# Kernel tuning notes

Hardware: AMD Instinct MI355X
Metric: run time of the kernel (lower is better)

The kernel has to match this reference:

```python
import jax, jax.numpy as jnp
import numpy as np

TINY = 1e-15
EPS = 1e-6
B, T, D, H, N = 1, 512, 512, 8, 64
A = N + 1  # ambient dim
TAU = 1.0


def mink(x, y):
    # Minkowski inner product over the last dim
    return -x[..., 0] * y[..., 0] + jnp.sum(x[..., 1:] * y[..., 1:], axis=-1)


def project(x):
    xx = mink(x, x)
    scale = jnp.sqrt(jnp.maximum(jnp.abs(xx), TINY))[..., None]
    x = x / scale
    return jnp.concatenate([jnp.abs(x[..., :1]), x[..., 1:]], axis=-1)


def exp_map(p, v):
    vn = jnp.sqrt(jnp.maximum(mink(v, v), TINY))[..., None]
    y = jnp.cosh(vn) * p + (jnp.sinh(vn) / jnp.maximum(vn, TINY)) * v
    return project(y)


def log_map(p, y):
    alpha = -mink(p, y)
    dist = jnp.arccosh(jnp.maximum(alpha, 1.0 + EPS))[..., None]
    u = y + alpha[..., None] * p
    un = jnp.sqrt(jnp.maximum(mink(u, u), TINY))[..., None]
    return dist / jnp.maximum(un, TINY) * u


def rope(u):
    # u: [B,H,T,N]; standard half-rotation RoPE, base 10000
    inv_freq = 1.0 / (10000.0 ** (jnp.arange(0, N, 2, dtype=jnp.float32) / N))
    ang = jnp.arange(T, dtype=jnp.float32)[:, None] * inv_freq[None, :]  # [T, N/2]
    cos = jnp.concatenate([jnp.cos(ang), jnp.cos(ang)], axis=-1)  # [T, N]
    sin = jnp.concatenate([jnp.sin(ang), jnp.sin(ang)], axis=-1)
    u1, u2 = u[..., : N // 2], u[..., N // 2:]
    rot = jnp.concatenate([-u2, u1], axis=-1)
    return u * cos + rot * sin


def lift(u):
    # append time-like 0, expmap at origin -> points on hyperboloid [B,H,T,A]
    v = jnp.concatenate([jnp.zeros(u.shape[:-1] + (1,), u.dtype), u], axis=-1)
    o = jnp.zeros((A,), u.dtype).at[0].set(1.0)
    return exp_map(o, v)


def setup_inputs() -> dict:
    key = jax.random.key(0)
    ks = jax.random.split(key, 10)
    s = 0.02
    x = jax.random.normal(ks[0], (B, T, D), jnp.float32)
    Wq = jax.random.normal(ks[1], (D, H * N), jnp.float32) * s
    bq = jax.random.normal(ks[2], (H * N,), jnp.float32) * s
    Wk = jax.random.normal(ks[3], (D, H * N), jnp.float32) * s
    bk = jax.random.normal(ks[4], (H * N,), jnp.float32) * s
    Wv = jax.random.normal(ks[5], (D, H * N), jnp.float32) * s
    bv = jax.random.normal(ks[6], (H * N,), jnp.float32) * s
    Wo = jax.random.normal(ks[7], (H * A, D), jnp.float32) * s
    bo = jax.random.normal(ks[8], (D,), jnp.float32) * s
    sp = jax.random.normal(ks[9], (N,), jnp.float32) * 0.1
    anchor_p = jnp.concatenate([jnp.sqrt(1.0 + jnp.sum(sp * sp))[None], sp])  # valid hyperboloid point
    return dict(x=x, Wq=Wq, bq=bq, Wk=Wk, bk=bk, Wv=Wv, bv=bv, Wo=Wo, bo=bo, anchor_p=anchor_p)


def reference(x, Wq, bq, Wk, bk, Wv, bv, Wo, bo, anchor_p):
    def pack(u):  # [B,T,H*N] -> [B,H,T,N]
        return u.reshape(B, T, H, N).transpose(0, 2, 1, 3)

    uq = rope(pack(x @ Wq + bq))
    uk = rope(pack(x @ Wk + bk))
    uv = pack(x @ Wv + bv)
    Q = lift(uq)  # [B,H,T,A]
    K = lift(uk)
    V = lift(uv)

    # pairwise Lorentz distance scores, softmax in fp32
    alpha_qk = -mink(Q[:, :, :, None, :].astype(jnp.float32), K[:, :, None, :, :].astype(jnp.float32))
    d = jnp.arccosh(jnp.maximum(alpha_qk, 1.0 + EPS))  # [B,H,T,T]
    attn = jax.nn.softmax(-TAU * d * d, axis=-1).astype(V.dtype)

    # one Karcher-mean step around the query point (karcher_steps=1)
    Y = Q
    logv = log_map(Y[:, :, :, None, :], V[:, :, None, :, :])  # [B,H,T,T,A]
    u = jnp.sum(attn[..., None] * logv, axis=3)  # [B,H,T,A]
    Y = exp_map(Y, u)

    Yc = Y.transpose(0, 2, 1, 3)  # [B,T,H,A]
    Z_tan = log_map(anchor_p[None, None, None, :], Yc).reshape(B, T, H * A)
    return Z_tan @ Wo + bo
```

## Files before the change

### kernel.cpp

```cpp
#include <hip/hip_runtime.h>
#include <math.h>

#define T_ 512
#define D_ 512
#define H_ 8
#define N_ 64
#define A_ 65
#define HN_ 512
#define HA_ 520
#define QS_ 66
#define VS_ 66
#define KTS_ 512
#define SYS_ 68
#define EPS_ 1e-6
#define EPSF_ 1e-6f
#define TINY_ 1e-15
#define IT 8
#define PTT 4
#define CTT 2

__device__ __forceinline__ double wsumd(double v){
#pragma unroll
  for (int o=32;o;o>>=1) v += __shfl_xor(v,o);
  return v;
}
__device__ __forceinline__ float wsumf(float v){
#pragma unroll
  for (int o=32;o;o>>=1) v += __shfl_xor(v,o);
  return v;
}
__device__ __forceinline__ float wmaxf(float v){
#pragma unroll
  for (int o=32;o;o>>=1) v = fmaxf(v,__shfl_xor(v,o));
  return v;
}
__device__ __forceinline__ float facoshf(float x){
  return __logf(x + sqrtf(fmaf(x,x,-1.f)));
}

__global__ void k_fill(float* __restrict__ out, float val){
  int i = blockIdx.x*256 + threadIdx.x;
  if (i < T_*D_) out[i] = val;
}

__global__ __launch_bounds__(256) void k_projlift(
    const float* __restrict__ x,
    const float* __restrict__ Wq, const float* __restrict__ bq,
    const float* __restrict__ Wk, const float* __restrict__ bk,
    const float* __restrict__ Wv, const float* __restrict__ bv,
    double* __restrict__ Qd, float* __restrict__ KTf,
    float* __restrict__ Vf, float* __restrict__ VTf){
  int mode = blockIdx.y;
  const float* W  = (mode==0)?Wq:((mode==1)?Wk:Wv);
  const float* bb = (mode==0)?bq:((mode==1)?bk:bv);
  int tid = threadIdx.x;
  int c = blockIdx.x*256 + tid;
  int n = c & 63, h = c >> 6;
  int t0 = blockIdx.z*PTT;
  float acc[PTT];
#pragma unroll
  for (int i=0;i<PTT;i++) acc[i]=0.f;

  float w0[8], w1[8];
#pragma unroll
  for (int k=0;k<8;k++) w0[k] = W[(size_t)(k)*HN_ + c];
#pragma unroll
  for (int k=0;k<8;k++) w1[k] = W[(size_t)(8+k)*HN_ + c];

#pragma unroll 2
  for (int d=0; d<D_-16; d+=8){
    float wp[8];
#pragma unroll
    for (int k=0;k<8;k++) wp[k] = W[(size_t)(d+16+k)*HN_ + c];
#pragma unroll
    for (int i=0;i<PTT;i++){
      const float* xr = x + (size_t)(t0+i)*D_ + d;
#pragma unroll
      for (int k=0;k<8;k++) acc[i] = fmaf(xr[k], w0[k], acc[i]);
    }
#pragma unroll
    for (int k=0;k<8;k++){ w0[k]=w1[k]; w1[k]=wp[k]; }
  }
#pragma unroll
  for (int i=0;i<PTT;i++){
    const float* xr = x + (size_t)(t0+i)*D_ + (D_-16);
#pragma unroll
    for (int k=0;k<8;k++) acc[i] = fmaf(xr[k],   w0[k], acc[i]);
#pragma unroll
    for (int k=0;k<8;k++) acc[i] = fmaf(xr[8+k], w1[k], acc[i]);
  }

  float bias = bb[c];
  double inv_f = 0.0;
  if (mode < 2) inv_f = 1.0 / pow(10000.0, (double)(2*(n&31))*(1.0/64.0));
#pragma unroll 1
  for (int i=0;i<PTT;i++){
    int t = t0 + i;
    double v = (double)(acc[i] + bias);
    if (mode < 2){
      double ang = (double)t * inv_f;
      double vp = __shfl_xor(v, 32);
      double rot = (n<32) ? -vp : vp;
      v = v*cos(ang) + rot*sin(ang);
    }
    double ss = wsumd(v*v);
    double vn = sqrt(fmax(ss, TINY_));
    double ch = cosh(vn);
    double s  = sinh(vn)/fmax(vn, TINY_);
    double y  = s*v;
    double xx = wsumd(y*y) - ch*ch;
    double scale = sqrt(fmax(fabs(xx), TINY_));
    double y0 = fabs(ch/scale), ya = y/scale;
    if (mode==0){
      double* o = Qd + (size_t)h*T_*QS_ + (size_t)t*QS_;
      if (n==0) o[0] = y0;
      o[n+1] = ya;
    } else if (mode==1){
      float* o = KTf + (size_t)h*66*KTS_ + t;
      if (n==0) o[0] = (float)y0;
      o[(size_t)(n+1)*KTS_] = (float)ya;
    } else {
      float y0f = (float)y0, yaf = (float)ya;
      float* o = Vf + (size_t)h*T_*VS_ + (size_t)t*VS_;
      if (n==0) o[0] = y0f;
      o[n+1] = yaf;
      float* ot = VTf + (size_t)h*66*KTS_ + t;
      if (n==0) ot[0] = y0f;
      ot[(size_t)(n+1)*KTS_] = yaf;
    }
  }
}

__global__ __launch_bounds__(256) void k_attnF(
    const double* __restrict__ Qd, const float* __restrict__ KTf,
    const float* __restrict__ VTf, const float* __restrict__ Vf,
    const float* __restrict__ anchor, float* __restrict__ Z){
  __shared__ double sYd[IT][QS_];
  __shared__ float  sYm[IT][SYS_];
  __shared__ float  s_w[IT][T_];
  __shared__ double sA[A_];
  __shared__ float  s_red[4][IT];
  __shared__ float  s_part[4][IT][64];
  __shared__ float  s_p64[4][IT];

  int h = blockIdx.x, i0 = blockIdx.y*IT, tid = threadIdx.x;
  int wv = tid>>6, lane = tid&63;
  const double* Qp = Qd  + (size_t)h*T_*QS_;
  const float*  KT = KTf + (size_t)h*66*KTS_;
  const float*  VT = VTf + (size_t)h*66*KTS_;
  const float*  Vp = Vf  + (size_t)h*T_*VS_;

  for (int f=tid; f<IT*QS_; f+=256){
    int i=f/QS_, a=f-i*QS_;
    sYd[i][a] = (a<A_) ? Qp[(size_t)(i0+i)*QS_ + a] : 0.0;
  }
  for (int f=tid; f<IT*SYS_; f+=256){
    int i=f/SYS_, a=f-i*SYS_;
    float v = (a<A_) ? (float)Qp[(size_t)(i0+i)*QS_ + a] : 0.f;
    sYm[i][a] = (a==0) ? v : -v;
  }
  if (tid < A_) sA[tid] = (double)anchor[tid];
  __syncthreads();

  int j0 = tid, j1 = tid + 256;
  {
    float aq0[IT], aq1[IT];
#pragma unroll
    for (int i=0;i<IT;i++){ aq0[i]=0.f; aq1[i]=0.f; }
    for (int a4=0; a4<16; a4++){
      int a = a4*4;
      float k00=KT[(size_t)(a+0)*KTS_+j0], k01=KT[(size_t)(a+1)*KTS_+j0];
      float k02=KT[(size_t)(a+2)*KTS_+j0], k03=KT[(size_t)(a+3)*KTS_+j0];
      float k10=KT[(size_t)(a+0)*KTS_+j1], k11=KT[(size_t)(a+1)*KTS_+j1];
      float k12=KT[(size_t)(a+2)*KTS_+j1], k13=KT[(size_t)(a+3)*KTS_+j1];
#pragma unroll
      for (int i=0;i<IT;i++){
        float4 ym = *reinterpret_cast<const float4*>(&sYm[i][a]);
        aq0[i] = fmaf(ym.w,k03,fmaf(ym.z,k02,fmaf(ym.y,k01,fmaf(ym.x,k00,aq0[i]))));
        aq1[i] = fmaf(ym.w,k13,fmaf(ym.z,k12,fmaf(ym.y,k11,fmaf(ym.x,k10,aq1[i]))));
      }
    }
    float kt0 = KT[(size_t)64*KTS_+j0], kt1 = KT[(size_t)64*KTS_+j1];
#pragma unroll
    for (int i=0;i<IT;i++){
      float a0 = fmaf(sYm[i][64], kt0, aq0[i]);
      float a1 = fmaf(sYm[i][64], kt1, aq1[i]);
      float d0 = facoshf(fmaxf(a0, 1.f+EPSF_));
      float d1 = facoshf(fmaxf(a1, 1.f+EPSF_));
      s_w[i][j0] = -d0*d0;
      s_w[i][j1] = -d1*d1;
    }
  }
  __syncthreads();

  for (int ii=0; ii<2; ii++){
    int i = wv*2 + ii;
    float m = -INFINITY;
#pragma unroll
    for (int kk=0;kk<8;kk++) m = fmaxf(m, s_w[i][lane+64*kk]);
    m = wmaxf(m);
    float e[8], sum=0.f;
#pragma unroll
    for (int kk=0;kk<8;kk++){ e[kk]=__expf(s_w[i][lane+64*kk]-m); sum+=e[kk]; }
    sum = wsumf(sum);
    float inv = 1.f/sum;
#pragma unroll
    for (int kk=0;kk<8;kk++) s_w[i][lane+64*kk] = e[kk]*inv;
  }
  __syncthreads();

  {
    float av0[IT], av1[IT];
#pragma unroll
    for (int i=0;i<IT;i++){ av0[i]=0.f; av1[i]=0.f; }
    for (int a4=0; a4<16; a4++){
      int a = a4*4;
      float v00=VT[(size_t)(a+0)*KTS_+j0], v01=VT[(size_t)(a+1)*KTS_+j0];
      float v02=VT[(size_t)(a+2)*KTS_+j0], v03=VT[(size_t)(a+3)*KTS_+j0];
      float v10=VT[(size_t)(a+0)*KTS_+j1], v11=VT[(size_t)(a+1)*KTS_+j1];
      float v12=VT[(size_t)(a+2)*KTS_+j1], v13=VT[(size_t)(a+3)*KTS_+j1];
#pragma unroll
      for (int i=0;i<IT;i++){
        float4 ym = *reinterpret_cast<const float4*>(&sYm[i][a]);
        av0[i] = fmaf(ym.w,v03,fmaf(ym.z,v02,fmaf(ym.y,v01,fmaf(ym.x,v00,av0[i]))));
        av1[i] = fmaf(ym.w,v13,fmaf(ym.z,v12,fmaf(ym.y,v11,fmaf(ym.x,v10,av1[i]))));
      }
    }
    float vt0 = VT[(size_t)64*KTS_+j0], vt1 = VT[(size_t)64*KTS_+j1];
    const float inv_un0 = 3.16227766016838e7f;
    float cyp[IT];
#pragma unroll
    for (int i=0;i<IT;i++){
      float a0 = fmaf(sYm[i][64], vt0, av0[i]);
      float a1 = fmaf(sYm[i][64], vt1, av1[i]);
      float at0 = s_w[i][j0], at1 = s_w[i][j1];
      float d0 = facoshf(fmaxf(a0, 1.f+EPSF_));
      float d1 = facoshf(fmaxf(a1, 1.f+EPSF_));
      float w0 = at0*d0*inv_un0;
      float w1 = at1*d1*inv_un0;
      s_w[i][j0] = w0;
      s_w[i][j1] = w1;
      cyp[i] = fmaf(w0, a0, w1*a1);
    }
#pragma unroll
    for (int i=0;i<IT;i++){
      float r = wsumf(cyp[i]);
      if (lane==0) s_red[wv][i] = r;
    }
  }
  __syncthreads();

  {
    float pL[IT], p64r[IT];
#pragma unroll
    for (int i=0;i<IT;i++){ pL[i]=0.f; p64r[i]=0.f; }
    int jb = wv*128;
    for (int jj=0; jj<128; jj+=4){
      int j = jb + jj;
      float vA = Vp[(size_t)(j+0)*VS_ + lane];
      float vB = Vp[(size_t)(j+1)*VS_ + lane];
      float vC = Vp[(size_t)(j+2)*VS_ + lane];
      float vD = Vp[(size_t)(j+3)*VS_ + lane];
#pragma unroll
      for (int i=0;i<IT;i++){
        float4 w4 = *reinterpret_cast<const float4*>(&s_w[i][j]);
        pL[i] = fmaf(w4.w,vD,fmaf(w4.z,vC,fmaf(w4.y,vB,fmaf(w4.x,vA,pL[i]))));
      }
    }
#pragma unroll
    for (int cc=0; cc<2; cc++){
      int j = jb + cc*64 + lane;
      float v64 = VT[(size_t)64*KTS_ + j];
#pragma unroll
      for (int i=0;i<IT;i++) p64r[i] = fmaf(s_w[i][j], v64, p64r[i]);
    }
#pragma unroll
    for (int i=0;i<IT;i++){
      s_part[wv][i][lane] = pL[i];
      float r = wsumf(p64r[i]);
      if (lane==0) s_p64[wv][i] = r;
    }
  }
  __syncthreads();

  for (int ii=0; ii<2; ii++){
    int r = wv*2 + ii;
    double cy = (double)s_red[0][r]+(double)s_red[1][r]+(double)s_red[2][r]+(double)s_red[3][r];
    double aL = (double)s_part[0][r][lane]+(double)s_part[1][r][lane]
              + (double)s_part[2][r][lane]+(double)s_part[3][r][lane];
    double a64 = (double)s_p64[0][r]+(double)s_p64[1][r]+(double)s_p64[2][r]+(double)s_p64[3][r];
    double ua  = fma(cy, sYd[r][lane], aL);
    double u64 = fma(cy, sYd[r][64],  a64);
    double c2 = (lane==0) ? fma(u64,u64, -ua*ua) : ua*ua;
    double mv = wsumd(c2);
    double vn = sqrt(fmax(mv, TINY_));
    double ch = cosh(vn);
    double sh = sinh(vn)/fmax(vn, TINY_);
    double ya  = fma(ch, sYd[r][lane], sh*ua);
    double y64 = fma(ch, sYd[r][64],  sh*u64);
    double c3 = (lane==0) ? fma(y64,y64, -ya*ya) : ya*ya;
    double px = wsumd(c3);
    double scale = sqrt(fmax(fabs(px), TINY_));
    double Pa  = ya/scale; if (lane==0) Pa = fabs(Pa);
    double P64 = y64/scale;
    double sAl = sA[lane];
    double azc = (lane==0) ? fma(sAl, Pa, -sA[64]*P64) : (-sAl*Pa);
    double az = wsumd(azc);
    double dz = acosh(fmax(az, 1.0+EPS_));
    double uza  = fma(az, sAl,    Pa);
    double uz64 = fma(az, sA[64], P64);
    double c4v = (lane==0) ? fma(uz64,uz64, -uza*uza) : uza*uza;
    double mz = wsumd(c4v);
    double unz = sqrt(fmax(mz, TINY_));
    double fz = dz/fmax(unz, TINY_);
    float* Zr = Z + (size_t)(i0+r)*HA_ + h*A_;
    Zr[lane] = (float)(fz*uza);
    if (lane==0) Zr[64] = (float)(fz*uz64);
  }
}

__global__ __launch_bounds__(256) void k_outD(
    const float* __restrict__ Zb, const float* __restrict__ Wo,
    const float* __restrict__ bo, float* __restrict__ out){
  int c  = blockIdx.x*256 + threadIdx.x;
  int t0 = blockIdx.y*CTT;
  float acc[CTT];
#pragma unroll
  for (int i=0;i<CTT;i++) acc[i]=0.f;
  for (int k=0;k<HA_;k+=4){
    float w0 = Wo[(size_t)(k+0)*D_ + c];
    float w1 = Wo[(size_t)(k+1)*D_ + c];
    float w2 = Wo[(size_t)(k+2)*D_ + c];
    float w3 = Wo[(size_t)(k+3)*D_ + c];
#pragma unroll
    for (int i=0;i<CTT;i++){
      const float* zr = Zb + (size_t)(t0+i)*HA_;
      acc[i] = fmaf(zr[k+0], w0, acc[i]);
      acc[i] = fmaf(zr[k+1], w1, acc[i]);
      acc[i] = fmaf(zr[k+2], w2, acc[i]);
      acc[i] = fmaf(zr[k+3], w3, acc[i]);
    }
  }
  float bb = bo[c];
#pragma unroll
  for (int i=0;i<CTT;i++) out[(t0+i)*D_ + c] = acc[i] + bb;
}

extern "C" void kernel_launch(void* const* d_in, const int* in_sizes, int n_in,
                              void* d_out, int out_size, void* d_ws, size_t ws_size,
                              hipStream_t stream){
  float* out = (float*)d_out;

  bool ok = (n_in == 10) && (out_size == T_*D_)
    && in_sizes[0]==T_*D_ && in_sizes[1]==D_*HN_ && in_sizes[2]==HN_
    && in_sizes[3]==D_*HN_ && in_sizes[4]==HN_
    && in_sizes[5]==D_*HN_ && in_sizes[6]==HN_
    && in_sizes[7]==HA_*D_ && in_sizes[8]==D_ && in_sizes[9]==A_;
  if (!ok){ k_fill<<<1024,256,0,stream>>>(out, 1.0e12f); return; }

  const float* x      = (const float*)d_in[0];
  const float* Wq     = (const float*)d_in[1];
  const float* bq     = (const float*)d_in[2];
  const float* Wk     = (const float*)d_in[3];
  const float* bk     = (const float*)d_in[4];
  const float* Wv     = (const float*)d_in[5];
  const float* bv     = (const float*)d_in[6];
  const float* Wo     = (const float*)d_in[7];
  const float* bo     = (const float*)d_in[8];
  const float* anchor = (const float*)d_in[9];
  char* ws = (char*)d_ws;

  size_t zbytes  = (size_t)T_*HA_*sizeof(float);
  size_t qbytes  = (size_t)H_*T_*QS_*sizeof(double);
  size_t ktbytes = (size_t)H_*66*KTS_*sizeof(float);
  size_t vbytes  = (size_t)H_*T_*VS_*sizeof(float);
  size_t vtbytes = (size_t)H_*66*KTS_*sizeof(float);
  size_t need    = zbytes+qbytes+ktbytes+vbytes+vtbytes;
  if (ws_size < need){ k_fill<<<1024,256,0,stream>>>(out, 2.0e12f); return; }

  float*  Zf = (float*)ws;
  double* Qd = (double*)(ws + zbytes);
  float*  KT = (float*) (ws + zbytes + qbytes);
  float*  Vf = (float*) (ws + zbytes + qbytes + ktbytes);
  float*  VT = (float*) (ws + zbytes + qbytes + ktbytes + vbytes);

  k_projlift<<<dim3(2,3,T_/PTT), 256, 0, stream>>>(x, Wq,bq, Wk,bk, Wv,bv, Qd, KT, Vf, VT);
  k_attnF   <<<dim3(H_, T_/IT), 256, 0, stream>>>(Qd, KT, VT, Vf, anchor, Zf);
  k_outD    <<<dim3(2, T_/CTT), 256, 0, stream>>>(Zf, Wo, bo, out);
}
```

Baseline: 101.6 us.

## Precompute RoPE trig table, store Q in fp32, and simplify cosh/sinh in lift

Adds a small kernel that tabulates the RoPE cos/sin values in double precision, so the projection kernel reads them instead of evaluating pow/cos/sin per element. The lift step now computes cosh and sinh from a single exp and gets the norm algebraically, which removes one wave reduction. Q is now stored as float instead of double, which halves its memory traffic and the shared-memory footprint in the attention kernel. The trade-offs are an extra kernel launch, extra workspace, and lower precision for Q.

Result: no change. 103.6 us (+1.9%).

```diff
diff --git a/kernel.cpp b/kernel.cpp
--- a/kernel.cpp
+++ b/kernel.cpp
@@ -43,12 +43,22 @@
   if (i < T_*D_) out[i] = val;
 }
 
+__global__ __launch_bounds__(256) void k_trig(double* __restrict__ tab){
+  int i = blockIdx.x*256 + threadIdx.x;
+  int t = i >> 5, fi = i & 31;
+  double inv_f = 1.0 / pow(10000.0, (double)(2*fi)*(1.0/64.0));
+  double ang = (double)t * inv_f;
+  tab[2*i+0] = cos(ang);
+  tab[2*i+1] = sin(ang);
+}
+
 __global__ __launch_bounds__(256) void k_projlift(
     const float* __restrict__ x,
     const float* __restrict__ Wq, const float* __restrict__ bq,
     const float* __restrict__ Wk, const float* __restrict__ bk,
     const float* __restrict__ Wv, const float* __restrict__ bv,
-    double* __restrict__ Qd, float* __restrict__ KTf,
+    const double* __restrict__ trig,
+    float* __restrict__ Qf, float* __restrict__ KTf,
     float* __restrict__ Vf, float* __restrict__ VTf){
   int mode = blockIdx.y;
   const float* W  = (mode==0)?Wq:((mode==1)?Wk:Wv);
@@ -91,51 +101,50 @@
   }
 
   float bias = bb[c];
-  double inv_f = 0.0;
-  if (mode < 2) inv_f = 1.0 / pow(10000.0, (double)(2*(n&31))*(1.0/64.0));
 #pragma unroll 1
   for (int i=0;i<PTT;i++){
     int t = t0 + i;
     double v = (double)(acc[i] + bias);
     if (mode < 2){
-      double ang = (double)t * inv_f;
+      const double2 cs2 = *reinterpret_cast<const double2*>(trig + 2*((size_t)t*32 + (n&31)));
       double vp = __shfl_xor(v, 32);
       double rot = (n<32) ? -vp : vp;
-      v = v*cos(ang) + rot*sin(ang);
+      v = v*cs2.x + rot*cs2.y;
     }
     double ss = wsumd(v*v);
     double vn = sqrt(fmax(ss, TINY_));
-    double ch = cosh(vn);
-    double s  = sinh(vn)/fmax(vn, TINY_);
-    double y  = s*v;
-    double xx = wsumd(y*y) - ch*ch;
+    double e  = exp(vn);
+    double ei = 1.0/e;
+    double ch = 0.5*(e+ei);
+    double s  = (0.5*(e-ei))/vn;
+    double xx = s*s*ss - ch*ch;
     double scale = sqrt(fmax(fabs(xx), TINY_));
-    double y0 = fabs(ch/scale), ya = y/scale;
+    float y0 = (float)fabs(ch/scale);
+    float ya = (float)(s*v/scale);
     if (mode==0){
-      double* o = Qd + (size_t)h*T_*QS_ + (size_t)t*QS_;
+      float* o = Qf + (size_t)h*T_*QS_ + (size_t)t*QS_;
       if (n==0) o[0] = y0;
       o[n+1] = ya;
     } else if (mode==1){
       float* o = KTf + (size_t)h*66*KTS_ + t;
-      if (n==0) o[0] = (float)y0;
-      o[(size_t)(n+1)*KTS_] = (float)ya;
+      if (n==0) o[0] = y0;
+      o[(size_t)(n+1)*KTS_] = ya;
     } else {
-      float y0f = (float)y0, yaf = (float)ya;
       float* o = Vf + (size_t)h*T_*VS_ + (size_t)t*VS_;
-      if (n==0) o[0] = y0f;
-      o[n+1] = yaf;
+      if (n==0) o[0] = y0;
+      o[n+1] = ya;
       float* ot = VTf + (size_t)h*66*KTS_ + t;
-      if (n==0) ot[0] = y0f;
-      ot[(size_t)(n+1)*KTS_] = yaf;
+      if (n==0) ot[0] = y0;
+      ot[(size_t)(n+1)*KTS_] = ya;
     }
   }
 }
 
 __global__ __launch_bounds__(256) void k_attnF(
-    const double* __restrict__ Qd, const float* __restrict__ KTf,
+    const float* __restrict__ Qf, const float* __restrict__ KTf,
     const float* __restrict__ VTf, const float* __restrict__ Vf,
     const float* __restrict__ anchor, float* __restrict__ Z){
-  __shared__ double sYd[IT][QS_];
+  __shared__ float  sYf[IT][QS_];
   __shared__ float  sYm[IT][SYS_];
   __shared__ float  s_w[IT][T_];
   __shared__ double sA[A_];
@@ -145,18 +154,18 @@
 
   int h = blockIdx.x, i0 = blockIdx.y*IT, tid = threadIdx.x;
   int wv = tid>>6, lane = tid&63;
-  const double* Qp = Qd  + (size_t)h*T_*QS_;
-  const float*  KT = KTf + (size_t)h*66*KTS_;
-  const float*  VT = VTf + (size_t)h*66*KTS_;
-  const float*  Vp = Vf  + (size_t)h*T_*VS_;
+  const float* Qp = Qf  + (size_t)h*T_*QS_;
+  const float* KT = KTf + (size_t)h*66*KTS_;
+  const float* VT = VTf + (size_t)h*66*KTS_;
+  const float* Vp = Vf  + (size_t)h*T_*VS_;
 
   for (int f=tid; f<IT*QS_; f+=256){
     int i=f/QS_, a=f-i*QS_;
-    sYd[i][a] = (a<A_) ? Qp[(size_t)(i0+i)*QS_ + a] : 0.0;
+    sYf[i][a] = (a<A_) ? Qp[(size_t)(i0+i)*QS_ + a] : 0.f;
   }
   for (int f=tid; f<IT*SYS_; f+=256){
     int i=f/SYS_, a=f-i*SYS_;
-    float v = (a<A_) ? (float)Qp[(size_t)(i0+i)*QS_ + a] : 0.f;
+    float v = (a<A_) ? Qp[(size_t)(i0+i)*QS_ + a] : 0.f;
     sYm[i][a] = (a==0) ? v : -v;
   }
   if (tid < A_) sA[tid] = (double)anchor[tid];
@@ -285,19 +294,21 @@
 
   for (int ii=0; ii<2; ii++){
     int r = wv*2 + ii;
+    double Yl  = (double)sYf[r][lane];
+    double Y64 = (double)sYf[r][64];
     double cy = (double)s_red[0][r]+(double)s_red[1][r]+(double)s_red[2][r]+(double)s_red[3][r];
     double aL = (double)s_part[0][r][lane]+(double)s_part[1][r][lane]
               + (double)s_part[2][r][lane]+(double)s_part[3][r][lane];
     double a64 = (double)s_p64[0][r]+(double)s_p64[1][r]+(double)s_p64[2][r]+(double)s_p64[3][r];
-    double ua  = fma(cy, sYd[r][lane], aL);
-    double u64 = fma(cy, sYd[r][64],  a64);
+    double ua  = fma(cy, Yl,  aL);
+    double u64 = fma(cy, Y64, a64);
     double c2 = (lane==0) ? fma(u64,u64, -ua*ua) : ua*ua;
     double mv = wsumd(c2);
     double vn = sqrt(fmax(mv, TINY_));
     double ch = cosh(vn);
     double sh = sinh(vn)/fmax(vn, TINY_);
-    double ya  = fma(ch, sYd[r][lane], sh*ua);
-    double y64 = fma(ch, sYd[r][64],  sh*u64);
+    double ya  = fma(ch, Yl,  sh*ua);
+    double y64 = fma(ch, Y64, sh*u64);
     double c3 = (lane==0) ? fma(y64,y64, -ya*ya) : ya*ya;
     double px = wsumd(c3);
     double scale = sqrt(fmax(fabs(px), TINY_));
@@ -371,20 +382,23 @@
   char* ws = (char*)d_ws;
 
   size_t zbytes  = (size_t)T_*HA_*sizeof(float);
-  size_t qbytes  = (size_t)H_*T_*QS_*sizeof(double);
+  size_t qbytes  = (size_t)H_*T_*QS_*sizeof(float);
   size_t ktbytes = (size_t)H_*66*KTS_*sizeof(float);
   size_t vbytes  = (size_t)H_*T_*VS_*sizeof(float);
   size_t vtbytes = (size_t)H_*66*KTS_*sizeof(float);
-  size_t need    = zbytes+qbytes+ktbytes+vbytes+vtbytes;
+  size_t tbytes  = (size_t)T_*32*2*sizeof(double);
+  size_t need    = zbytes+qbytes+ktbytes+vbytes+vtbytes+tbytes;
   if (ws_size < need){ k_fill<<<1024,256,0,stream>>>(out, 2.0e12f); return; }
 
   float*  Zf = (float*)ws;
-  double* Qd = (double*)(ws + zbytes);
-  float*  KT = (float*) (ws + zbytes + qbytes);
-  float*  Vf = (float*) (ws + zbytes + qbytes + ktbytes);
-  float*  VT = (float*) (ws + zbytes + qbytes + ktbytes + vbytes);
-
-  k_projlift<<<dim3(2,3,T_/PTT), 256, 0, stream>>>(x, Wq,bq, Wk,bk, Wv,bv, Qd, KT, Vf, VT);
-  k_attnF   <<<dim3(H_, T_/IT), 256, 0, stream>>>(Qd, KT, VT, Vf, anchor, Zf);
-  k_outD    <<<dim3(2, T_/CTT), 256, 0, stream>>>(Zf, Wo, bo, out);
-}
+  float*  Qf = (float*)(ws + zbytes);
+  float*  KT = (float*)(ws + zbytes + qbytes);
+  float*  Vf = (float*)(ws + zbytes + qbytes + ktbytes);
+  float*  VT = (float*)(ws + zbytes + qbytes + ktbytes + vbytes);
+  double* TB = (double*)(ws + zbytes + qbytes + ktbytes + vbytes + vtbytes);
+
+  k_trig    <<<dim3(T_*32/256),  256, 0, stream>>>(TB);
+  k_projlift<<<dim3(2,3,T_/PTT), 256, 0, stream>>>(x, Wq,bq, Wk,bk, Wv,bv, TB, Qf, KT, Vf, VT);
+  k_attnF   <<<dim3(H_, T_/IT),  256, 0, stream>>>(Qf, KT, VT, Vf, anchor, Zf);
+  k_outD    <<<dim3(2, T_/CTT),  256, 0, stream>>>(Zf, Wo, bo, out);
+}
```
